# Optimization experiments

Hardware: AMD Instinct MI355X
Metric: run time of the kernel (lower is better)

The kernel has to match this reference:

```python
import jax, jax.numpy as jnp
import numpy as np

KS = 3            # kernel_size
DILS = (1, 2, 4)  # dilation_list == padding_list
EPS = 1e-5        # BN eps


def _unfold3(x, d):
    # emulate F.unfold(kernel=3, dilation=d, padding=d, stride=1).view(b, c, 9, h, w)
    b, c, h, w = x.shape
    xp = jnp.pad(x, ((0, 0), (0, 0), (d, d), (d, d)))
    pats = [xp[:, :, i * d:i * d + h, j * d:j * d + w] for i in range(KS) for j in range(KS)]
    return jnp.stack(pats, axis=2)


def _conv1x1(x, w, b):
    return jnp.einsum('bchw,oc->bohw', x, w) + b[None, :, None, None]


def _bn_relu(x, g, be, m, v):
    s = g / jnp.sqrt(v + EPS)
    return jax.nn.relu(x * s[None, :, None, None] + (be - m * s)[None, :, None, None])


def _proj(x, w1, b1, g1, be1, m1, v1, w2, b2, g2, be2, m2, v2):
    h = _bn_relu(_conv1x1(x, w1, b1), g1, be1, m1, v1)
    return _bn_relu(_conv1x1(h, w2, b2), g2, be2, m2, v2)


def setup_inputs():
    key = jax.random.key(0)
    Cin, Ck, Cv, Cout = 512, 256, 256, 512
    B, H, W = 4, 64, 64
    ks = iter(jax.random.split(key, 48))

    def nrm(shape, s=0.02):
        return jax.random.normal(next(ks), shape, jnp.float32) * s

    def bn(c):
        return (jnp.ones((c,), jnp.float32) + nrm((c,), 0.1),  # gamma
                nrm((c,), 0.1),                                 # beta
                nrm((c,), 0.1),                                 # running mean
                jax.random.uniform(next(ks), (c,), jnp.float32, 0.5, 1.5))  # running var

    inp = {"x": jax.random.normal(next(ks), (B, Cin, H, W), jnp.float32)}
    for p in ("k", "q"):
        g1, be1, m1, v1 = bn(Ck)
        g2, be2, m2, v2 = bn(Ck)
        inp.update({
            p + "1_w": nrm((Ck, Cin)), p + "1_b": nrm((Ck,)),
            p + "1_g": g1, p + "1_be": be1, p + "1_m": m1, p + "1_v": v1,
            p + "2_w": nrm((Ck, Ck)), p + "2_b": nrm((Ck,)),
            p + "2_g": g2, p + "2_be": be2, p + "2_m": m2, p + "2_v": v2,
        })
    inp["v_w"] = nrm((Cv, Cin)); inp["v_b"] = nrm((Cv,))
    inp["w_w"] = nrm((Cout, Cv)); inp["w_b"] = nrm((Cout,))
    return inp


def reference(x,
              k1_w, k1_b, k1_g, k1_be, k1_m, k1_v,
              k2_w, k2_b, k2_g, k2_be, k2_m, k2_v,
              q1_w, q1_b, q1_g, q1_be, q1_m, q1_v,
              q2_w, q2_b, q2_g, q2_be, q2_m, q2_v,
              v_w, v_b, w_w, w_b):
    # scale == 1: MaxPool2d(1x1-equivalent) and final bilinear resize are identities.
    value = _conv1x1(x, v_w, v_b)                                  # (b,cv,h,w)
    keyf = _proj(x, k1_w, k1_b, k1_g, k1_be, k1_m, k1_v,
                 k2_w, k2_b, k2_g, k2_be, k2_m, k2_v)              # (b,ck,h,w)
    query = _proj(x, q1_w, q1_b, q1_g, q1_be, q1_m, q1_v,
                  q2_w, q2_b, q2_g, q2_be, q2_m, q2_v)             # (b,ck,h,w)
    uk = jnp.concatenate([_unfold3(keyf, d) for d in DILS], axis=2)   # (b,ck,27,h,w)
    uv = jnp.concatenate([_unfold3(value, d) for d in DILS], axis=2)  # (b,cv,27,h,w)
    sim = jnp.sum(uk * query[:, :, None], axis=1, keepdims=True)      # (b,1,27,h,w)
    sim = jax.nn.softmax(sim, axis=2)
    context = jnp.sum(sim * uv, axis=2)                               # (b,cv,h,w)
    return _conv1x1(context, w_w, w_b)
```

## Files before the change

### kernel.cpp

```cpp
#include <hip/hip_runtime.h>

#define HW   4096
#define Hh   64
#define Ww   64
#define NB   27
#define EPSBN 1e-5f

typedef _Float16 f16x8 __attribute__((ext_vector_type(8)));
typedef _Float16 f16x4 __attribute__((ext_vector_type(4)));
typedef _Float16 f16x2 __attribute__((ext_vector_type(2)));
typedef float    f32x4 __attribute__((ext_vector_type(4)));

__device__ __forceinline__ void gld_lds16(const void* g, void* l) {
    __builtin_amdgcn_global_load_lds(
        (const __attribute__((address_space(1))) unsigned int*)g,
        (__attribute__((address_space(3))) unsigned int*)l, 16, 0, 0);
}

__global__ __launch_bounds__(256)
void prep_kernel(const float* s0, const float* s1, const float* s2,
                 const float* s3, const float* s4, const float* s5,
                 _Float16* d0, _Float16* d1, _Float16* d2,
                 _Float16* d3, _Float16* d4, _Float16* d5)
{
    const int bid = blockIdx.x;
    const int j  = bid >> 6;
    const int bx = bid & 63;
    const float* s = j==0?s0: j==1?s1: j==2?s2: j==3?s3: j==4?s4: s5;
    _Float16*  d = j==0?d0: j==1?d1: j==2?d2: j==3?d3: j==4?d4: d5;
    const int  n = (j==3 || j==4) ? 65536 : 131072;
    const int  i = (bx * 256 + threadIdx.x) * 8;
    if (i < n) {
        f16x8 h;
        #pragma unroll
        for (int k = 0; k < 8; ++k) h[k] = (_Float16)s[i + k];
        *(f16x8*)(d + i) = h;
    }
}

struct GJob {
    const _Float16* in;
    const float*    xf;
    const _Float16* w;
    const float* b; const float* g; const float* be; const float* m; const float* v;
    _Float16* oh;
    float*    of;
};

__global__ __launch_bounds__(256)
void gemm64(GJob J0, GJob J1, GJob J2, int nmb0, int nmb01, int nmbTot,
            int K, int JO, int mode)
{
    __shared__ _Float16 As[64 * 64];
    __shared__ _Float16 Bs[128 * 64];

    const int tid  = threadIdx.x;
    const int lane = tid & 63;
    const int w    = tid >> 6;
    const int lr   = lane & 15;
    const int lg   = lane >> 4;
    const int wm   = w & 1;
    const int wn   = w >> 1;

    const int bid = blockIdx.x;
    const int xcd = bid & 7;
    const int jj  = bid >> 3;
    const int nb  = xcd * 16 + jj / nmbTot;
    const int mb  = jj % nmbTot;

    const bool i0 = mb < nmb0;
    const bool i1 = !i0 && mb < nmb01;
#define SELJ(f) (i0 ? J0.f : (i1 ? J1.f : J2.f))
    const _Float16* Jin = SELJ(in);
    const float*    Jxf = SELJ(xf);
    const _Float16* Jw  = SELJ(w);
    const float* Jb  = SELJ(b);
    const float* Jg  = SELJ(g);
    const float* Jbe = SELJ(be);
    const float* Jm  = SELJ(m);
    const float* Jv  = SELJ(v);
    _Float16* Joh = SELJ(oh);
    float*    Jof = SELJ(of);
#undef SELJ
    const int obase = (mb - (i0 ? 0 : (i1 ? nmb0 : nmb01))) * 64;

    const int scol = (((lane & 7) ^ (lane >> 3)) << 3);
    const int rowA = w * 16 + (lane >> 3);
    const _Float16* aSrc = Jw + (size_t)(obase + rowA) * K + scol;
    const int rowB = w * 32 + (lane >> 3);
    const _Float16* bSrc = Jin ? (Jin + (size_t)(nb * 128 + rowB) * K + scol) : nullptr;

    const int xrow = tid & 127;
    const int chq  = tid >> 7;
    const float* xbase = nullptr;
    if (Jxf) {
        const int bb = nb >> 5;
        const int pp = (nb & 31) * 128 + xrow;
        xbase = Jxf + (size_t)bb * 512 * HW + pp;
    }
    const int bxorw = (xrow & 7) << 4;

    f32x4 acc[2][4] = {};
    const int nr = K >> 6;

    for (int rd = 0; rd < nr; ++rd) {
        const int kb = rd * 64;
        __syncthreads();
        gld_lds16(aSrc + kb,                  (char*)As + w * 2048);
        gld_lds16(aSrc + (size_t)8 * K + kb,  (char*)As + w * 2048 + 1024);
        if (Jxf) {
            float fr[32];
            #pragma unroll
            for (int g2 = 0; g2 < 4; ++g2)
                #pragma unroll
                for (int i2 = 0; i2 < 8; ++i2)
                    fr[g2 * 8 + i2] = xbase[(size_t)(kb + chq * 32 + g2 * 8 + i2) * HW];
            #pragma unroll
            for (int g2 = 0; g2 < 4; ++g2) {
                f16x8 hv;
                #pragma unroll
                for (int i2 = 0; i2 < 8; ++i2) hv[i2] = (_Float16)fr[g2 * 8 + i2];
                *(f16x8*)((char*)Bs + xrow * 128 + ((chq * 64 + g2 * 16) ^ bxorw)) = hv;
            }
        } else {
            #pragma unroll
            for (int j2 = 0; j2 < 4; ++j2)
                gld_lds16(bSrc + (size_t)j2 * 8 * K + kb, (char*)Bs + w * 4096 + j2 * 1024);
        }
        __syncthreads();

        #pragma unroll
        for (int ks = 0; ks < 2; ++ks) {
            const int colx = (ks * 64 + lg * 16) ^ ((lr & 7) << 4);
            f16x8 afr[2], bfr[4];
            afr[0] = *(const f16x8*)((const char*)As + (wm * 32 + lr) * 128 + colx);
            afr[1] = *(const f16x8*)((const char*)As + (wm * 32 + 16 + lr) * 128 + colx);
            #pragma unroll
            for (int t = 0; t < 4; ++t)
                bfr[t] = *(const f16x8*)((const char*)Bs + (wn * 64 + t * 16 + lr) * 128 + colx);
            #pragma unroll
            for (int ai = 0; ai < 2; ++ai)
                #pragma unroll
                for (int bj = 0; bj < 4; ++bj)
                    acc[ai][bj] = __builtin_amdgcn_mfma_f32_16x16x32_f16(
                        afr[ai], bfr[bj], acc[ai][bj], 0, 0, 0);
        }
    }

    const int relu = (Jg != nullptr);
    #pragma unroll
    for (int ai = 0; ai < 2; ++ai) {
        const int o4 = obase + wm * 32 + ai * 16 + lg * 4;
        float sc[4], of_[4];
        #pragma unroll
        for (int r = 0; r < 4; ++r) {
            const int o = o4 + r;
            if (Jg) { float s = Jg[o] * rsqrtf(Jv[o] + EPSBN); sc[r] = s; of_[r] = fmaf(Jb[o] - Jm[o], s, Jbe[o]); }
            else    { sc[r] = 1.f; of_[r] = Jb[o]; }
        }
        #pragma unroll
        for (int bj = 0; bj < 4; ++bj) {
            const int pg = nb * 128 + wn * 64 + bj * 16 + lr;
            float vv[4];
            #pragma unroll
            for (int r = 0; r < 4; ++r) {
                float t = fmaf(acc[ai][bj][r], sc[r], of_[r]);
                vv[r] = relu ? fmaxf(t, 0.f) : t;
            }
            if (mode == 0) {
                f16x4 hh;
                #pragma unroll
                for (int r = 0; r < 4; ++r) hh[r] = (_Float16)vv[r];
                *(f16x4*)(Joh + (size_t)pg * JO + o4) = hh;
            } else {
                #pragma unroll
                for (int r = 0; r < 4; ++r)
                    Jof[((size_t)(pg >> 12) * JO + o4 + r) * HW + (pg & 4095)] = vv[r];
            }
        }
    }
}

__global__ __launch_bounds__(256)
void attn_fused(const _Float16* __restrict__ keyT, const _Float16* __restrict__ qryT,
                const _Float16* __restrict__ valT, _Float16* __restrict__ ctxT)
{
    const int tid  = threadIdx.x;
    const int slot = tid & 31;
    const int b    = blockIdx.y;
    const int p    = blockIdx.x * 8 + (tid >> 5);
    const int y    = p >> 6;
    const int xc   = p & 63;

    int   idx[NB];
    float valf[NB];
    #pragma unroll
    for (int n = 0; n < NB; ++n) {
        const int d  = (n < 9) ? 1 : (n < 18 ? 2 : 4);
        const int i  = (n / 3) % 3 - 1;
        const int j  = n % 3 - 1;
        const int yy = y + i * d, xx = xc + j * d;
        const bool ok = ((unsigned)yy < (unsigned)Hh) && ((unsigned)xx < (unsigned)Ww);
        idx[n]  = min(max(yy, 0), Hh - 1) * Ww + min(max(xx, 0), Ww - 1);
        valf[n] = ok ? 1.f : 0.f;
    }

    const size_t base = (size_t)b * HW * 256 + slot * 8;
    const f16x8 q8 = *(const f16x8*)(qryT + base + (size_t)p * 256);

    f16x2 qp[4];
    qp[0] = __builtin_shufflevector(q8, q8, 0, 1);
    qp[1] = __builtin_shufflevector(q8, q8, 2, 3);
    qp[2] = __builtin_shufflevector(q8, q8, 4, 5);
    qp[3] = __builtin_shufflevector(q8, q8, 6, 7);

    float sim[NB];
    #pragma unroll
    for (int n = 0; n < NB; ++n) {
        const f16x8 k8 = *(const f16x8*)(keyT + base + (size_t)idx[n] * 256);
        float s = 0.f;
        s = __builtin_amdgcn_fdot2(__builtin_shufflevector(k8, k8, 0, 1), qp[0], s, false);
        s = __builtin_amdgcn_fdot2(__builtin_shufflevector(k8, k8, 2, 3), qp[1], s, false);
        s = __builtin_amdgcn_fdot2(__builtin_shufflevector(k8, k8, 4, 5), qp[2], s, false);
        s = __builtin_amdgcn_fdot2(__builtin_shufflevector(k8, k8, 6, 7), qp[3], s, false);
        sim[n] = s;
    }

    #pragma unroll
    for (int n = 0; n < NB; ++n) {
        float s = sim[n];
        s += __shfl_xor(s, 1);
        s += __shfl_xor(s, 2);
        s += __shfl_xor(s, 4);
        s += __shfl_xor(s, 8);
        s += __shfl_xor(s, 16);
        sim[n] = s * valf[n];
    }

    float mx = sim[0];
    #pragma unroll
    for (int n = 1; n < NB; ++n) mx = fmaxf(mx, sim[n]);
    float sum = 0.f;
    #pragma unroll
    for (int n = 0; n < NB; ++n) { sim[n] = __expf(sim[n] - mx); sum += sim[n]; }
    const float inv = 1.f / sum;
    #pragma unroll
    for (int n = 0; n < NB; ++n) sim[n] = sim[n] * inv * valf[n];

    float acc[8];
    #pragma unroll
    for (int i = 0; i < 8; ++i) acc[i] = 0.f;
    #pragma unroll
    for (int n = 0; n < NB; ++n) {
        const f16x8 v8 = *(const f16x8*)(valT + base + (size_t)idx[n] * 256);
        const float w = sim[n];
        #pragma unroll
        for (int i = 0; i < 8; ++i) acc[i] = fmaf(w, (float)v8[i], acc[i]);
    }

    f16x8 h;
    #pragma unroll
    for (int i = 0; i < 8; ++i) h[i] = (_Float16)acc[i];
    *(f16x8*)(ctxT + base + (size_t)p * 256) = h;
}

extern "C" void kernel_launch(void* const* d_in, const int* in_sizes, int n_in,
                              void* d_out, int out_size, void* d_ws, size_t ws_size,
                              hipStream_t stream)
{
    (void)in_sizes; (void)n_in; (void)out_size; (void)ws_size;
    const float* x     = (const float*)d_in[0];
    const float* k1_w  = (const float*)d_in[1];
    const float* k1_b  = (const float*)d_in[2];
    const float* k1_g  = (const float*)d_in[3];
    const float* k1_be = (const float*)d_in[4];
    const float* k1_m  = (const float*)d_in[5];
    const float* k1_v  = (const float*)d_in[6];
    const float* k2_w  = (const float*)d_in[7];
    const float* k2_b  = (const float*)d_in[8];
    const float* k2_g  = (const float*)d_in[9];
    const float* k2_be = (const float*)d_in[10];
    const float* k2_m  = (const float*)d_in[11];
    const float* k2_v  = (const float*)d_in[12];
    const float* q1_w  = (const float*)d_in[13];
    const float* q1_b  = (const float*)d_in[14];
    const float* q1_g  = (const float*)d_in[15];
    const float* q1_be = (const float*)d_in[16];
    const float* q1_m  = (const float*)d_in[17];
    const float* q1_v  = (const float*)d_in[18];
    const float* q2_w  = (const float*)d_in[19];
    const float* q2_b  = (const float*)d_in[20];
    const float* q2_g  = (const float*)d_in[21];
    const float* q2_be = (const float*)d_in[22];
    const float* q2_m  = (const float*)d_in[23];
    const float* q2_v  = (const float*)d_in[24];
    const float* v_w   = (const float*)d_in[25];
    const float* v_b   = (const float*)d_in[26];
    const float* w_w   = (const float*)d_in[27];
    const float* w_b   = (const float*)d_in[28];

    _Float16* hw = (_Float16*)d_ws;
    const size_t SH = (size_t)4 * HW * 256;
    _Float16* wv_h  = hw;
    _Float16* wk1_h = wv_h  + 131072;
    _Float16* wq1_h = wk1_h + 131072;
    _Float16* wk2_h = wq1_h + 131072;
    _Float16* wq2_h = wk2_h + 65536;
    _Float16* ww_h  = wq2_h + 65536;
    _Float16* k1T   = ww_h  + 131072;
    _Float16* q1T   = k1T + SH;
    _Float16* valT  = q1T + SH;
    _Float16* ctxT  = valT + SH;
    _Float16* keyPC = ctxT + SH;
    _Float16* qryPC = keyPC + SH;

    prep_kernel<<<384, 256, 0, stream>>>(v_w, k1_w, q1_w, k2_w, q2_w, w_w,
                                         wv_h, wk1_h, wq1_h, wk2_h, wq2_h, ww_h);

    GJob jv  = { nullptr, x, wv_h,  v_b,  nullptr, nullptr, nullptr, nullptr, valT,  nullptr };
    GJob jk1 = { nullptr, x, wk1_h, k1_b, k1_g, k1_be, k1_m, k1_v,            k1T,   nullptr };
    GJob jq1 = { nullptr, x, wq1_h, q1_b, q1_g, q1_be, q1_m, q1_v,            q1T,   nullptr };
    GJob jk2 = { k1T, nullptr, wk2_h, k2_b, k2_g, k2_be, k2_m, k2_v,          keyPC, nullptr };
    GJob jq2 = { q1T, nullptr, wq2_h, q2_b, q2_g, q2_be, q2_m, q2_v,          qryPC, nullptr };
    GJob jw  = { ctxT, nullptr, ww_h, w_b,  nullptr, nullptr, nullptr, nullptr, nullptr, (float*)d_out };

    gemm64<<<1536, 256, 0, stream>>>(jv, jk1, jq1, 4, 8, 12, 512, 256, 0);
    gemm64<<<1024, 256, 0, stream>>>(jk2, jq2, jq2, 4, 8, 8, 256, 256, 0);
    attn_fused<<<dim3(512, 4), 256, 0, stream>>>(keyPC, qryPC, valT, ctxT);
    gemm64<<<1024, 256, 0, stream>>>(jw, jw, jw, 8, 8, 8, 256, 512, 2);
}
```

Measured before the change: 103.9 us.

## Share B tile across three projections per block and prefetch fp32 x loads

Replaces the 256-thread 64x128 GEMM with a 512-thread kernel where each block computes up to three 64-row output tiles (value, key1, query1) against one shared 128-pixel B tile. The fp32 input x is converted and staged into LDS only once for all three projections, instead of once per job. The next round's x loads are issued into registers before the MFMA work so they overlap with compute. This trades more LDS and registers per block, and fewer total blocks, for less redundant global traffic on x.

```diff
diff --git a/kernel.cpp b/kernel.cpp
--- a/kernel.cpp
+++ b/kernel.cpp
@@ -47,138 +47,163 @@
     float*    of;
 };
 
-__global__ __launch_bounds__(256)
-void gemm64(GJob J0, GJob J1, GJob J2, int nmb0, int nmb01, int nmbTot,
-            int K, int JO, int mode)
+__global__ __launch_bounds__(512)
+void gemm_f(GJob J0, GJob J1, GJob J2, int stage, int K, int JO, int mode)
 {
-    __shared__ _Float16 As[64 * 64];
+    __shared__ _Float16 As[3 * 64 * 64];
     __shared__ _Float16 Bs[128 * 64];
 
     const int tid  = threadIdx.x;
     const int lane = tid & 63;
-    const int w    = tid >> 6;
+    const int w8   = tid >> 6;
     const int lr   = lane & 15;
     const int lg   = lane >> 4;
-    const int wm   = w & 1;
-    const int wn   = w >> 1;
+    const int wm   = w8 & 3;
+    const int wn   = w8 >> 2;
 
     const int bid = blockIdx.x;
     const int xcd = bid & 7;
     const int jj  = bid >> 3;
-    const int nb  = xcd * 16 + jj / nmbTot;
-    const int mb  = jj % nmbTot;
-
-    const bool i0 = mb < nmb0;
-    const bool i1 = !i0 && mb < nmb01;
-#define SELJ(f) (i0 ? J0.f : (i1 ? J1.f : J2.f))
-    const _Float16* Jin = SELJ(in);
-    const float*    Jxf = SELJ(xf);
-    const _Float16* Jw  = SELJ(w);
-    const float* Jb  = SELJ(b);
-    const float* Jg  = SELJ(g);
-    const float* Jbe = SELJ(be);
-    const float* Jm  = SELJ(m);
-    const float* Jv  = SELJ(v);
-    _Float16* Joh = SELJ(oh);
-    float*    Jof = SELJ(of);
-#undef SELJ
-    const int obase = (mb - (i0 ? 0 : (i1 ? nmb0 : nmb01))) * 64;
+    const int nb  = xcd * 16 + (jj >> 2);
+    const int u   = jj & 3;
+
+    const int nA = (stage == 1) ? 3 : 2;
+    int js0, js1, js2, ob0, ob1, ob2;
+    if (stage == 1)      { js0 = 0; js1 = 1; js2 = 2; ob0 = ob1 = ob2 = u * 64; }
+    else if (stage == 2) { js0 = js1 = js2 = (u >> 1); ob0 = (u & 1) * 128; ob1 = ob0 + 64; ob2 = ob1; }
+    else                 { js0 = js1 = js2 = 0; ob0 = u * 128; ob1 = ob0 + 64; ob2 = ob1; }
+
+#define JSEL(js, f) ((js) == 0 ? J0.f : ((js) == 1 ? J1.f : J2.f))
+    const _Float16* w0 = JSEL(js0, w);
+    const _Float16* w1 = JSEL(js1, w);
+    const _Float16* w2 = JSEL(js2, w);
+    const float* b0 = JSEL(js0, b); const float* g0 = JSEL(js0, g);
+    const float* be0 = JSEL(js0, be); const float* m0 = JSEL(js0, m); const float* v0 = JSEL(js0, v);
+    const float* b1 = JSEL(js1, b); const float* g1 = JSEL(js1, g);
+    const float* be1 = JSEL(js1, be); const float* m1 = JSEL(js1, m); const float* v1 = JSEL(js1, v);
+    const float* b2 = JSEL(js2, b); const float* g2 = JSEL(js2, g);
+    const float* be2 = JSEL(js2, be); const float* m2 = JSEL(js2, m); const float* v2 = JSEL(js2, v);
+    _Float16* oh0 = JSEL(js0, oh); float* of0 = JSEL(js0, of);
+    _Float16* oh1 = JSEL(js1, oh); float* of1 = JSEL(js1, of);
+    _Float16* oh2 = JSEL(js2, oh); float* of2 = JSEL(js2, of);
+    const _Float16* bIn = JSEL(js0, in);
+    const float*    bXf = JSEL(js0, xf);
+#undef JSEL
 
     const int scol = (((lane & 7) ^ (lane >> 3)) << 3);
-    const int rowA = w * 16 + (lane >> 3);
-    const _Float16* aSrc = Jw + (size_t)(obase + rowA) * K + scol;
-    const int rowB = w * 32 + (lane >> 3);
-    const _Float16* bSrc = Jin ? (Jin + (size_t)(nb * 128 + rowB) * K + scol) : nullptr;
-
-    const int xrow = tid & 127;
-    const int chq  = tid >> 7;
-    const float* xbase = nullptr;
-    if (Jxf) {
-        const int bb = nb >> 5;
-        const int pp = (nb & 31) * 128 + xrow;
-        xbase = Jxf + (size_t)bb * 512 * HW + pp;
-    }
+    const int rowA = w8 * 8 + (lane >> 3);
+    const _Float16* aS0 = w0 + (size_t)(ob0 + rowA) * K + scol;
+    const _Float16* aS1 = w1 + (size_t)(ob1 + rowA) * K + scol;
+    const _Float16* aS2 = w2 + (size_t)(ob2 + rowA) * K + scol;
+
+    const int rowB = w8 * 16 + (lane >> 3);
+    const _Float16* bS = bIn ? (bIn + (size_t)(nb * 128 + rowB) * K + scol) : nullptr;
+
+    const int xrow  = tid & 127;
+    const int chq   = tid >> 7;
+    const int pgS   = nb * 128 + xrow;
+    const float* xbase = bXf ? (bXf + ((size_t)(pgS >> 12) * 512) * HW + (pgS & 4095)) : nullptr;
     const int bxorw = (xrow & 7) << 4;
-
-    f32x4 acc[2][4] = {};
+    const bool f32B = (bXf != nullptr);
+
+    float fr[16];
+    auto ISSUE_BX = [&](int rd) {
+        const int cb = rd * 64 + chq * 16;
+        #pragma unroll
+        for (int i2 = 0; i2 < 16; ++i2)
+            fr[i2] = xbase[(size_t)(cb + i2) * HW];
+    };
+    auto WRITE_BX = [&]() {
+        #pragma unroll
+        for (int g4 = 0; g4 < 2; ++g4) {
+            f16x8 hv;
+            #pragma unroll
+            for (int i2 = 0; i2 < 8; ++i2) hv[i2] = (_Float16)fr[g4 * 8 + i2];
+            *(f16x8*)((char*)Bs + xrow * 128 + ((chq * 32 + g4 * 16) ^ bxorw)) = hv;
+        }
+    };
+
+    f32x4 acc0[4] = {}, acc1[4] = {}, acc2[4] = {};
     const int nr = K >> 6;
+
+    if (f32B) ISSUE_BX(0);
 
     for (int rd = 0; rd < nr; ++rd) {
         const int kb = rd * 64;
         __syncthreads();
-        gld_lds16(aSrc + kb,                  (char*)As + w * 2048);
-        gld_lds16(aSrc + (size_t)8 * K + kb,  (char*)As + w * 2048 + 1024);
-        if (Jxf) {
-            float fr[32];
-            #pragma unroll
-            for (int g2 = 0; g2 < 4; ++g2)
-                #pragma unroll
-                for (int i2 = 0; i2 < 8; ++i2)
-                    fr[g2 * 8 + i2] = xbase[(size_t)(kb + chq * 32 + g2 * 8 + i2) * HW];
-            #pragma unroll
-            for (int g2 = 0; g2 < 4; ++g2) {
-                f16x8 hv;
-                #pragma unroll
-                for (int i2 = 0; i2 < 8; ++i2) hv[i2] = (_Float16)fr[g2 * 8 + i2];
-                *(f16x8*)((char*)Bs + xrow * 128 + ((chq * 64 + g2 * 16) ^ bxorw)) = hv;
-            }
+        if (f32B) {
+            WRITE_BX();
         } else {
-            #pragma unroll
-            for (int j2 = 0; j2 < 4; ++j2)
-                gld_lds16(bSrc + (size_t)j2 * 8 * K + kb, (char*)Bs + w * 4096 + j2 * 1024);
+            gld_lds16(bS + kb,                 (char*)Bs + w8 * 2048);
+            gld_lds16(bS + (size_t)8 * K + kb, (char*)Bs + w8 * 2048 + 1024);
         }
+        gld_lds16(aS0 + kb, (char*)As + w8 * 1024);
+        gld_lds16(aS1 + kb, (char*)As + 8192 + w8 * 1024);
+        if (nA > 2) gld_lds16(aS2 + kb, (char*)As + 16384 + w8 * 1024);
         __syncthreads();
+        if (f32B && rd + 1 < nr) ISSUE_BX(rd + 1);
 
         #pragma unroll
         for (int ks = 0; ks < 2; ++ks) {
             const int colx = (ks * 64 + lg * 16) ^ ((lr & 7) << 4);
-            f16x8 afr[2], bfr[4];
-            afr[0] = *(const f16x8*)((const char*)As + (wm * 32 + lr) * 128 + colx);
-            afr[1] = *(const f16x8*)((const char*)As + (wm * 32 + 16 + lr) * 128 + colx);
+            const int arow = (wm * 16 + lr) * 128 + colx;
+            f16x8 bfr[4];
             #pragma unroll
             for (int t = 0; t < 4; ++t)
                 bfr[t] = *(const f16x8*)((const char*)Bs + (wn * 64 + t * 16 + lr) * 128 + colx);
+            const f16x8 af0 = *(const f16x8*)((const char*)As + arow);
+            const f16x8 af1 = *(const f16x8*)((const char*)As + 8192 + arow);
             #pragma unroll
-            for (int ai = 0; ai < 2; ++ai)
+            for (int bj = 0; bj < 4; ++bj)
+                acc0[bj] = __builtin_amdgcn_mfma_f32_16x16x32_f16(af0, bfr[bj], acc0[bj], 0, 0, 0);
+            #pragma unroll
+            for (int bj = 0; bj < 4; ++bj)
+                acc1[bj] = __builtin_amdgcn_mfma_f32_16x16x32_f16(af1, bfr[bj], acc1[bj], 0, 0, 0);
+            if (nA > 2) {
+                const f16x8 af2 = *(const f16x8*)((const char*)As + 16384 + arow);
                 #pragma unroll
                 for (int bj = 0; bj < 4; ++bj)
-                    acc[ai][bj] = __builtin_amdgcn_mfma_f32_16x16x32_f16(
-                        afr[ai], bfr[bj], acc[ai][bj], 0, 0, 0);
-        }
-    }
-
-    const int relu = (Jg != nullptr);
-    #pragma unroll
-    for (int ai = 0; ai < 2; ++ai) {
-        const int o4 = obase + wm * 32 + ai * 16 + lg * 4;
-        float sc[4], of_[4];
-        #pragma unroll
-        for (int r = 0; r < 4; ++r) {
-            const int o = o4 + r;
-            if (Jg) { float s = Jg[o] * rsqrtf(Jv[o] + EPSBN); sc[r] = s; of_[r] = fmaf(Jb[o] - Jm[o], s, Jbe[o]); }
-            else    { sc[r] = 1.f; of_[r] = Jb[o]; }
-        }
-        #pragma unroll
-        for (int bj = 0; bj < 4; ++bj) {
-            const int pg = nb * 128 + wn * 64 + bj * 16 + lr;
-            float vv[4];
-            #pragma unroll
-            for (int r = 0; r < 4; ++r) {
-                float t = fmaf(acc[ai][bj][r], sc[r], of_[r]);
-                vv[r] = relu ? fmaxf(t, 0.f) : t;
-            }
-            if (mode == 0) {
-                f16x4 hh;
-                #pragma unroll
-                for (int r = 0; r < 4; ++r) hh[r] = (_Float16)vv[r];
-                *(f16x4*)(Joh + (size_t)pg * JO + o4) = hh;
-            } else {
-                #pragma unroll
-                for (int r = 0; r < 4; ++r)
-                    Jof[((size_t)(pg >> 12) * JO + o4 + r) * HW + (pg & 4095)] = vv[r];
+                    acc2[bj] = __builtin_amdgcn_mfma_f32_16x16x32_f16(af2, bfr[bj], acc2[bj], 0, 0, 0);
             }
         }
     }
+
+#define EPI(accS, obS, bS_, gS, beS, mS, vS, ohS, ofS) do {                      \
+        const int o4 = (obS) + wm * 16 + lg * 4;                                 \
+        float sc[4], off[4];                                                     \
+        _Pragma("unroll")                                                        \
+        for (int r = 0; r < 4; ++r) {                                            \
+            const int o = o4 + r;                                                \
+            if (gS) { float s = (gS)[o] * rsqrtf((vS)[o] + EPSBN);               \
+                      sc[r] = s; off[r] = fmaf((bS_)[o] - (mS)[o], s, (beS)[o]); }\
+            else    { sc[r] = 1.f; off[r] = (bS_)[o]; }                          \
+        }                                                                        \
+        _Pragma("unroll")                                                        \
+        for (int bj = 0; bj < 4; ++bj) {                                         \
+            const int pg = nb * 128 + wn * 64 + bj * 16 + lr;                    \
+            float vv[4];                                                         \
+            _Pragma("unroll")                                                    \
+            for (int r = 0; r < 4; ++r) {                                        \
+                float t = fmaf(accS[bj][r], sc[r], off[r]);                      \
+                vv[r] = (gS) ? fmaxf(t, 0.f) : t;                                \
+            }                                                                    \
+            if (mode == 0) {                                                     \
+                f16x4 hh;                                                        \
+                _Pragma("unroll")                                                \
+                for (int r = 0; r < 4; ++r) hh[r] = (_Float16)vv[r];             \
+                *(f16x4*)((ohS) + (size_t)pg * JO + o4) = hh;                    \
+            } else {                                                             \
+                _Pragma("unroll")                                                \
+                for (int r = 0; r < 4; ++r)                                      \
+                    (ofS)[((size_t)(pg >> 12) * JO + o4 + r) * HW + (pg & 4095)] = vv[r]; \
+            }                                                                    \
+        }                                                                        \
+    } while (0)
+
+    EPI(acc0, ob0, b0, g0, be0, m0, v0, oh0, of0);
+    EPI(acc1, ob1, b1, g1, be1, m1, v1, oh1, of1);
+    if (nA > 2) EPI(acc2, ob2, b2, g2, be2, m2, v2, oh2, of2);
+#undef EPI
 }
 
 __global__ __launch_bounds__(256)
@@ -324,8 +349,8 @@
     GJob jq2 = { q1T, nullptr, wq2_h, q2_b, q2_g, q2_be, q2_m, q2_v,          qryPC, nullptr };
     GJob jw  = { ctxT, nullptr, ww_h, w_b,  nullptr, nullptr, nullptr, nullptr, nullptr, (float*)d_out };
 
-    gemm64<<<1536, 256, 0, stream>>>(jv, jk1, jq1, 4, 8, 12, 512, 256, 0);
-    gemm64<<<1024, 256, 0, stream>>>(jk2, jq2, jq2, 4, 8, 8, 256, 256, 0);
+    gemm_f<<<512, 512, 0, stream>>>(jv, jk1, jq1, 1, 512, 256, 0);
+    gemm_f<<<512, 512, 0, stream>>>(jk2, jq2, jq2, 2, 256, 256, 0);
     attn_fused<<<dim3(512, 4), 256, 0, stream>>>(keyPC, qryPC, valT, ctxT);
-    gemm64<<<1024, 256, 0, stream>>>(jw, jw, jw, 8, 8, 8, 256, 512, 2);
-}
+    gemm_f<<<512, 512, 0, stream>>>(jw, jw, jw, 4, 256, 512, 2);
+}
```

After: 86.91 us. 1.2x faster.
